# Performance work log

Hardware: AMD Instinct MI355X
Metric: run time of the kernel (lower is better)

## Reference

```python
import jax, jax.numpy as jnp
import numpy as np

TOP_K = 2  # num_activated_experts

def setup_inputs() -> dict:
    key = jax.random.key(0)
    kx, kg, k1, k2, k3 = jax.random.split(key, 5)
    B, S, H, I, E = 2, 2048, 1024, 2048, 8
    scale = 0.02
    return {
        "x": jax.random.normal(kx, (B, S, H), dtype=jnp.float32),
        "gate_w": jax.random.normal(kg, (E, H), dtype=jnp.float32) * scale,   # router Linear weight [E,H]
        "w_gate": jax.random.normal(k1, (E, H, I), dtype=jnp.float32) * scale, # gate_proj per expert
        "w_up":   jax.random.normal(k2, (E, H, I), dtype=jnp.float32) * scale, # up_proj per expert
        "w_down": jax.random.normal(k3, (E, I, H), dtype=jnp.float32) * scale, # down_proj per expert
    }

def reference(x, gate_w, w_gate, w_up, w_down):
    B, S, H = x.shape
    E = gate_w.shape[0]
    T = B * S
    xf = x.reshape(T, H)
    # router
    router_logits = xf @ gate_w.T                                  # [T,E]
    probs = jax.nn.softmax(router_logits.astype(jnp.float32), axis=-1)
    top_w, top_i = jax.lax.top_k(probs, TOP_K)                      # [T,K]
    top_w = top_w / jnp.sum(top_w, axis=-1, keepdims=True)
    top_w = top_w.astype(x.dtype)
    # dense combine weights: w[t,e] = routing weight if expert e selected, else 0
    w = jnp.zeros((T, E), dtype=x.dtype).at[jnp.arange(T)[:, None], top_i].add(top_w)
    # experts (SwiGLU), computed densely over experts, masked by combine weights
    g = jnp.einsum('th,ehi->tei', xf, w_gate)                       # [T,E,I]
    u = jnp.einsum('th,ehi->tei', xf, w_up)                         # [T,E,I]
    h = jax.nn.silu(g) * u
    y = jnp.einsum('tei,eih->teh', h, w_down)                       # [T,E,H]
    out = jnp.einsum('teh,te->th', y, w)                            # weighted combine
    return out.reshape(B, S, H), router_logits
```

## Files before the change

kernel.cpp:

```cpp
#include <hip/hip_runtime.h>
#include <hip/hip_bf16.h>
#include <math.h>

#define T_TOK 4096
#define H_DIM 1024
#define I_DIM 2048
#define E_NUM 8

typedef __bf16 bf16x8 __attribute__((ext_vector_type(8)));
typedef float  f32x4  __attribute__((ext_vector_type(4)));
typedef unsigned short u16x4 __attribute__((ext_vector_type(4)));
typedef unsigned short u16x8 __attribute__((ext_vector_type(8)));

__device__ inline void gll16(const void* g, void* l) {
    __builtin_amdgcn_global_load_lds(
        (const __attribute__((address_space(1))) void*)g,
        (__attribute__((address_space(3))) void*)l, 16, 0, 0);
}

__device__ inline unsigned short f2bf(float f) {
    union { float f; unsigned u; } v; v.f = f;
    unsigned r = v.u + 0x7FFF + ((v.u >> 16) & 1);
    return (unsigned short)(r >> 16);
}

__device__ inline void stage_tile64(const unsigned short* gbase, size_t stride_elems,
                                    int k0, char* smbase, int tid, int wv) {
#pragma unroll
    for (int it = 0; it < 4; ++it) {
        int idx = it * 256 + tid;
        int r   = idx >> 3;
        int kg  = (idx & 7) ^ (r & 7);
        const void* g = gbase + (size_t)r * stride_elems + k0 + kg * 8;
        void* l = smbase + it * 4096 + wv * 1024;
        gll16(g, l);
    }
}

__device__ inline bf16x8 frag_ld64(const char* smbase, int row, int kg_log) {
    int kg = kg_log ^ (row & 7);
    return *(const bf16x8*)(smbase + row * 128 + kg * 16);
}

__global__ __launch_bounds__(256) void router_kernel(
    const float* __restrict__ x, const float* __restrict__ gw,
    float* __restrict__ logits_out, int* __restrict__ te, float2* __restrict__ tw)
{
    int wave = threadIdx.x >> 6;
    int lane = threadIdx.x & 63;
    int t = blockIdx.x * 4 + wave;
    if (t >= T_TOK) return;

    float xs[16];
#pragma unroll
    for (int i = 0; i < 16; ++i) xs[i] = x[(size_t)t * H_DIM + i * 64 + lane];

    float lg[E_NUM];
#pragma unroll
    for (int e = 0; e < E_NUM; ++e) {
        float acc = 0.f;
#pragma unroll
        for (int i = 0; i < 16; ++i) acc += xs[i] * gw[e * H_DIM + i * 64 + lane];
#pragma unroll
        for (int off = 32; off >= 1; off >>= 1) acc += __shfl_xor(acc, off, 64);
        lg[e] = acc;
    }

    if (lane == 0) {
#pragma unroll
        for (int e = 0; e < E_NUM; ++e) logits_out[(size_t)t * E_NUM + e] = lg[e];
        float m = lg[0];
        for (int e = 1; e < E_NUM; ++e) m = fmaxf(m, lg[e]);
        float p[E_NUM]; float s = 0.f;
        for (int e = 0; e < E_NUM; ++e) { p[e] = expf(lg[e] - m); s += p[e]; }
        float invs = 1.f / s;
        for (int e = 0; e < E_NUM; ++e) p[e] *= invs;
        int i0 = 0; float p0 = p[0];
        for (int e = 1; e < E_NUM; ++e) if (p[e] > p0) { p0 = p[e]; i0 = e; }
        int i1 = -1; float p1 = -1.f;
        for (int e = 0; e < E_NUM; ++e) { if (e == i0) continue; if (p[e] > p1) { p1 = p[e]; i1 = e; } }
        float inv = 1.f / (p0 + p1);
        te[t] = i0 | (i1 << 4);
        tw[t] = make_float2(p0 * inv, p1 * inv);
    }
}

__global__ __launch_bounds__(256) void scan_kernel(
    const int* __restrict__ te, const float2* __restrict__ tw,
    int* __restrict__ counts, int* __restrict__ tok_list,
    float* __restrict__ w_list, int* __restrict__ tslot)
{
    int e = blockIdx.x;
    int tid = threadIdx.x, lane = tid & 63, wv = tid >> 6;

    int    pk[16];
    float2 w2[16];
#pragma unroll
    for (int c = 0; c < 16; ++c) pk[c] = te[c * 256 + tid];
#pragma unroll
    for (int c = 0; c < 16; ++c) w2[c] = tw[c * 256 + tid];

    __shared__ int wbase[4];
    int running = 0;
#pragma unroll
    for (int c = 0; c < 16; ++c) {
        int t  = c * 256 + tid;
        int e0 = pk[c] & 15, e1 = pk[c] >> 4;
        bool f0 = (e0 == e), f1 = (e1 == e);
        bool f  = f0 || f1;
        unsigned long long b = __ballot(f);
        int pre = __popcll(b & ((1ull << lane) - 1ull));
        if (lane == 0) wbase[wv] = __popcll(b);
        __syncthreads();
        int base = running;
#pragma unroll
        for (int w = 0; w < 4; ++w) if (w < wv) base += wbase[w];
        int tot = wbase[0] + wbase[1] + wbase[2] + wbase[3];
        if (f) {
            int pos = base + pre;
            tok_list[e * T_TOK + pos] = t;
            w_list[e * T_TOK + pos]   = f0 ? w2[c].x : w2[c].y;
            tslot[t * 2 + (f0 ? 0 : 1)] = e * T_TOK + pos;
        }
        running += tot;
        __syncthreads();
    }
    if (tid == 0) counts[e] = running;
}

__global__ void offsets_kernel(const int* __restrict__ counts, int* __restrict__ poff)
{
    if (threadIdx.x == 0 && blockIdx.x == 0) {
        int s = 0;
        for (int e = 0; e < E_NUM; ++e) { poff[e] = s; s += ((counts[e] + 127) >> 7) << 7; }
    }
}

__global__ __launch_bounds__(256) void gather_x(
    const float* __restrict__ x, const int* __restrict__ counts,
    const int* __restrict__ poff, const int* __restrict__ tok_list,
    unsigned short* __restrict__ xg)
{
    int e  = blockIdx.x >> 7;
    int mt = blockIdx.x & 127;
    int cnt = counts[e];
    int padded = (cnt + 127) & ~127;
    int m0 = mt * 32;
    if (m0 >= padded) return;
    int base = poff[e];
#pragma unroll 4
    for (int it = 0; it < 32; ++it) {
        int idx = it * 256 + threadIdx.x;
        int r  = idx >> 8;
        int c4 = idx & 255;
        int m  = m0 + r;
        int mc = (m < cnt) ? m : cnt - 1;
        int t  = tok_list[e * T_TOK + mc];
        float4 v = *(const float4*)(x + (size_t)t * H_DIM + c4 * 4);
        u16x4 o;
        o[0] = f2bf(v.x); o[1] = f2bf(v.y); o[2] = f2bf(v.z); o[3] = f2bf(v.w);
        *(u16x4*)(xg + (size_t)(base + m) * H_DIM + c4 * 4) = o;
    }
}

__global__ __launch_bounds__(256) void transpose_cvt(
    const float* __restrict__ in, unsigned short* __restrict__ out, int K, int N)
{
    int e = blockIdx.z;
    in  += (size_t)e * K * N;
    out += (size_t)e * K * N;
    int k0 = blockIdx.y * 64, n0 = blockIdx.x * 64;
    __shared__ float t[64][65];
#pragma unroll
    for (int it = 0; it < 4; ++it) {
        int idx = it * 256 + threadIdx.x;
        int r = idx >> 4, c4 = idx & 15;
        float4 v = *(const float4*)(in + (size_t)(k0 + r) * N + n0 + c4 * 4);
        t[r][c4 * 4 + 0] = v.x; t[r][c4 * 4 + 1] = v.y;
        t[r][c4 * 4 + 2] = v.z; t[r][c4 * 4 + 3] = v.w;
    }
    __syncthreads();
#pragma unroll
    for (int it = 0; it < 2; ++it) {
        int slot = it * 256 + threadIdx.x;
        int n = slot >> 3, kg = slot & 7;
        u16x8 o;
#pragma unroll
        for (int j = 0; j < 8; ++j) o[j] = f2bf(t[kg * 8 + j][n]);
        *(u16x8*)(out + (size_t)(n0 + n) * K + k0 + kg * 8) = o;
    }
}

__global__ __launch_bounds__(256, 2) void mlp1_kernel(
    const unsigned short* __restrict__ xg,
    const unsigned short* __restrict__ wgT, const unsigned short* __restrict__ wuT,
    const int* __restrict__ counts, const int* __restrict__ poff,
    unsigned short* __restrict__ hbuf)
{
    int e = blockIdx.z;
    int cnt = counts[e];
    int m0 = blockIdx.y * 128;
    if (m0 >= cnt) return;
    int n0 = blockIdx.x * 128;

    const unsigned short* A  = xg  + (size_t)(poff[e] + m0) * H_DIM;
    const unsigned short* Bg = wgT + (size_t)e * I_DIM * H_DIM + (size_t)n0 * H_DIM;
    const unsigned short* Bu = wuT + (size_t)e * I_DIM * H_DIM + (size_t)n0 * H_DIM;

    __shared__ char sm[49152];
    char* sA  = sm;
    char* sBg = sm + 16384;
    char* sBu = sm + 32768;

    int tid = threadIdx.x, lane = tid & 63, wv = tid >> 6;
    int wm = (wv >> 1) * 64, wn = (wv & 1) * 64;
    int q = lane >> 4, rl = lane & 15;

    f32x4 accg[4][4], accu[4][4];
#pragma unroll
    for (int i = 0; i < 4; ++i)
#pragma unroll
        for (int j = 0; j < 4; ++j) { accg[i][j] = (f32x4){0.f,0.f,0.f,0.f}; accu[i][j] = (f32x4){0.f,0.f,0.f,0.f}; }

    for (int k0 = 0; k0 < H_DIM; k0 += 64) {
        stage_tile64(A,  H_DIM, k0, sA,  tid, wv);
        stage_tile64(Bg, H_DIM, k0, sBg, tid, wv);
        stage_tile64(Bu, H_DIM, k0, sBu, tid, wv);
        __syncthreads();

#pragma unroll
        for (int h = 0; h < 2; ++h) {
            bf16x8 af[4], bgf[4], bu2[4];
#pragma unroll
            for (int i = 0; i < 4; ++i) af[i]  = frag_ld64(sA,  wm + i * 16 + rl, h * 4 + q);
#pragma unroll
            for (int j = 0; j < 4; ++j) { bgf[j] = frag_ld64(sBg, wn + j * 16 + rl, h * 4 + q);
                                          bu2[j] = frag_ld64(sBu, wn + j * 16 + rl, h * 4 + q); }
#pragma unroll
            for (int i = 0; i < 4; ++i)
#pragma unroll
                for (int j = 0; j < 4; ++j) {
                    accg[i][j] = __builtin_amdgcn_mfma_f32_16x16x32_bf16(af[i], bgf[j], accg[i][j], 0, 0, 0);
                    accu[i][j] = __builtin_amdgcn_mfma_f32_16x16x32_bf16(af[i], bu2[j], accu[i][j], 0, 0, 0);
                }
        }
        __syncthreads();
    }

    size_t hrow0 = (size_t)(poff[e] + m0);
#pragma unroll
    for (int i = 0; i < 4; ++i)
#pragma unroll
        for (int p = 0; p < 4; ++p) {
            int row = wm + i * 16 + q * 4 + p;
            unsigned short* orow = hbuf + (hrow0 + row) * I_DIM + n0 + wn + rl;
#pragma unroll
            for (int j = 0; j < 4; ++j) {
                float g = accg[i][j][p], u = accu[i][j][p];
                float hv = g / (1.f + __expf(-g)) * u;
                orow[j * 16] = f2bf(hv);
            }
        }
}

__global__ __launch_bounds__(256, 2) void mlp2_kernel(
    const unsigned short* __restrict__ hbuf,
    const unsigned short* __restrict__ wdT,
    const int* __restrict__ counts, const int* __restrict__ poff,
    float* __restrict__ ybuf)
{
    int e = blockIdx.z;
    int cnt = counts[e];
    int m0 = blockIdx.y * 128;
    if (m0 >= cnt) return;
    int n0 = blockIdx.x * 128;

    const unsigned short* A = hbuf + (size_t)(poff[e] + m0) * I_DIM;
    const unsigned short* B = wdT  + (size_t)e * H_DIM * I_DIM + (size_t)n0 * I_DIM;

    __shared__ char sm[32768];
    char* sA = sm;
    char* sB = sm + 16384;

    int tid = threadIdx.x, lane = tid & 63, wv = tid >> 6;
    int wm = (wv >> 1) * 64, wn = (wv & 1) * 64;
    int q = lane >> 4, rl = lane & 15;

    f32x4 acc[4][4];
#pragma unroll
    for (int i = 0; i < 4; ++i)
#pragma unroll
        for (int j = 0; j < 4; ++j) acc[i][j] = (f32x4){0.f,0.f,0.f,0.f};

    for (int k0 = 0; k0 < I_DIM; k0 += 64) {
        stage_tile64(A, I_DIM, k0, sA, tid, wv);
        stage_tile64(B, I_DIM, k0, sB, tid, wv);
        __syncthreads();

#pragma unroll
        for (int h = 0; h < 2; ++h) {
            bf16x8 af[4], bf[4];
#pragma unroll
            for (int i = 0; i < 4; ++i) af[i] = frag_ld64(sA, wm + i * 16 + rl, h * 4 + q);
#pragma unroll
            for (int j = 0; j < 4; ++j) bf[j] = frag_ld64(sB, wn + j * 16 + rl, h * 4 + q);
#pragma unroll
            for (int i = 0; i < 4; ++i)
#pragma unroll
                for (int j = 0; j < 4; ++j)
                    acc[i][j] = __builtin_amdgcn_mfma_f32_16x16x32_bf16(af[i], bf[j], acc[i][j], 0, 0, 0);
        }
        __syncthreads();
    }

    size_t yrow0 = (size_t)(poff[e] + m0);
#pragma unroll
    for (int i = 0; i < 4; ++i)
#pragma unroll
        for (int p = 0; p < 4; ++p) {
            int row = wm + i * 16 + q * 4 + p;
            float* op = ybuf + (yrow0 + row) * H_DIM + n0 + wn + rl;
#pragma unroll
            for (int j = 0; j < 4; ++j) op[j * 16] = acc[i][j][p];
        }
}

__global__ __launch_bounds__(256) void combine_kernel(
    const float* __restrict__ ybuf, const int* __restrict__ poff,
    const int* __restrict__ tslot, const float* __restrict__ w_list,
    float* __restrict__ out)
{
    int t  = blockIdx.x;
    int c4 = threadIdx.x;
    int s0 = tslot[t * 2 + 0], s1 = tslot[t * 2 + 1];
    float w0 = w_list[s0], w1 = w_list[s1];
    int e0 = s0 >> 12, p0 = s0 & 4095;
    int e1 = s1 >> 12, p1 = s1 & 4095;
    size_t r0 = (size_t)(poff[e0] + p0) * H_DIM;
    size_t r1 = (size_t)(poff[e1] + p1) * H_DIM;
    float4 a = *(const float4*)(ybuf + r0 + c4 * 4);
    float4 b = *(const float4*)(ybuf + r1 + c4 * 4);
    float4 o;
    o.x = w0 * a.x + w1 * b.x;
    o.y = w0 * a.y + w1 * b.y;
    o.z = w0 * a.z + w1 * b.z;
    o.w = w0 * a.w + w1 * b.w;
    *(float4*)(out + (size_t)t * H_DIM + c4 * 4) = o;
}

extern "C" void kernel_launch(void* const* d_in, const int* in_sizes, int n_in,
                              void* d_out, int out_size, void* d_ws, size_t ws_size,
                              hipStream_t stream)
{
    const float* x      = (const float*)d_in[0];
    const float* gate_w = (const float*)d_in[1];
    const float* w_gate = (const float*)d_in[2];
    const float* w_up   = (const float*)d_in[3];
    const float* w_down = (const float*)d_in[4];

    float* out        = (float*)d_out;
    float* logits_out = out + (size_t)T_TOK * H_DIM;

    char* ws = (char*)d_ws;
    int*   counts   = (int*)ws;
    int*   poff     = (int*)(ws + 64);
    int*   tok_list = (int*)(ws + 1024);
    float* w_list   = (float*)(ws + 1024 + E_NUM * T_TOK * 4);
    int*   tslot    = (int*)(ws + 1024 + 2 * E_NUM * T_TOK * 4);
    int*   te       = (int*)(ws + 1024 + 2 * E_NUM * T_TOK * 4 + 2 * T_TOK * 4);
    float2* tw      = (float2*)(ws + 1024 + 2 * E_NUM * T_TOK * 4 + 3 * T_TOK * 4);

    const size_t XG_ROWS = 9216;
    const size_t OFF_XG = 1u << 20;
    const size_t OFF_HB = OFF_XG + XG_ROWS * H_DIM * 2;
    const size_t OFF_WG = OFF_HB + XG_ROWS * I_DIM * 2;
    const size_t OFF_WU = OFF_WG + (size_t)E_NUM * H_DIM * I_DIM * 2;
    const size_t OFF_WD = OFF_WU + (size_t)E_NUM * H_DIM * I_DIM * 2;

    unsigned short* xg   = (unsigned short*)(ws + OFF_XG);
    unsigned short* hbuf = (unsigned short*)(ws + OFF_HB);
    unsigned short* wgT  = (unsigned short*)(ws + OFF_WG);
    unsigned short* wuT  = (unsigned short*)(ws + OFF_WU);
    unsigned short* wdT  = (unsigned short*)(ws + OFF_WD);
    float* ybuf = (float*)(ws + OFF_WG);

    router_kernel<<<T_TOK / 4, 256, 0, stream>>>(x, gate_w, logits_out, te, tw);
    scan_kernel<<<E_NUM, 256, 0, stream>>>(te, tw, counts, tok_list, w_list, tslot);
    offsets_kernel<<<1, 64, 0, stream>>>(counts, poff);

    dim3 gt1(I_DIM / 64, H_DIM / 64, E_NUM);
    transpose_cvt<<<gt1, 256, 0, stream>>>(w_gate, wgT, H_DIM, I_DIM);
    transpose_cvt<<<gt1, 256, 0, stream>>>(w_up,   wuT, H_DIM, I_DIM);
    dim3 gt2(H_DIM / 64, I_DIM / 64, E_NUM);
    transpose_cvt<<<gt2, 256, 0, stream>>>(w_down, wdT, I_DIM, H_DIM);

    gather_x<<<E_NUM * 128, 256, 0, stream>>>(x, counts, poff, tok_list, xg);

    dim3 g1(I_DIM / 128, T_TOK / 128, E_NUM);
    mlp1_kernel<<<g1, 256, 0, stream>>>(xg, wgT, wuT, counts, poff, hbuf);

    dim3 g2(H_DIM / 128, T_TOK / 128, E_NUM);
    mlp2_kernel<<<g2, 256, 0, stream>>>(hbuf, wdT, counts, poff, ybuf);

    combine_kernel<<<T_TOK, 256, 0, stream>>>(ybuf, poff, tslot, w_list, out);
}
```

Baseline: 417.2 us.

## Double-buffer LDS staging and widen expert GEMM tiles to 128x256 with 512 threads

Both expert GEMM kernels now use a two-stage LDS ping-pong with a K-step of 32. The next tile's global-to-LDS loads are issued before the MFMA work on the current tile, so load latency overlaps compute and only one barrier is needed per step. Block tiles grow from 128x128 to 128x256 with 8 waves, which raises reuse of the A tile. In exchange, LDS use is larger (80KB for mlp1), which may reduce occupancy, and the grid has fewer blocks, which may hurt load balance across the uneven per-expert counts.

Measured after the change: 440.5 us. 5.6% more time.

```diff
diff --git a/kernel.cpp b/kernel.cpp
--- a/kernel.cpp
+++ b/kernel.cpp
@@ -24,22 +24,26 @@
     return (unsigned short)(r >> 16);
 }
 
-__device__ inline void stage_tile64(const unsigned short* gbase, size_t stride_elems,
-                                    int k0, char* smbase, int tid, int wv) {
-#pragma unroll
-    for (int it = 0; it < 4; ++it) {
-        int idx = it * 256 + tid;
-        int r   = idx >> 3;
-        int kg  = (idx & 7) ^ (r & 7);
-        const void* g = gbase + (size_t)r * stride_elems + k0 + kg * 8;
-        void* l = smbase + it * 4096 + wv * 1024;
-        gll16(g, l);
-    }
-}
-
-__device__ inline bf16x8 frag_ld64(const char* smbase, int row, int kg_log) {
-    int kg = kg_log ^ (row & 7);
-    return *(const bf16x8*)(smbase + row * 128 + kg * 16);
+__device__ inline void stage_a32(const unsigned short* gbase, size_t stride, int k0,
+                                 char* dst, int tid, int wv) {
+    int r  = tid >> 2;
+    int kg = (tid & 3) ^ (r & 3);
+    gll16(gbase + (size_t)r * stride + k0 + kg * 8, dst + wv * 1024);
+}
+__device__ inline void stage_b32(const unsigned short* gbase, size_t stride, int k0,
+                                 char* dst, int tid, int wv) {
+#pragma unroll
+    for (int it = 0; it < 2; ++it) {
+        int idx = it * 512 + tid;
+        int r  = idx >> 2;
+        int kg = (idx & 3) ^ (r & 3);
+        gll16(gbase + (size_t)r * stride + k0 + kg * 8, dst + it * 8192 + wv * 1024);
+    }
+}
+
+__device__ inline bf16x8 frag_ld32(const char* smbase, int row, int q) {
+    int kg = q ^ (row & 3);
+    return *(const bf16x8*)(smbase + row * 64 + kg * 16);
 }
 
 __global__ __launch_bounds__(256) void router_kernel(
@@ -191,7 +195,7 @@
     }
 }
 
-__global__ __launch_bounds__(256, 2) void mlp1_kernel(
+__global__ __launch_bounds__(512, 2) void mlp1_kernel(
     const unsigned short* __restrict__ xg,
     const unsigned short* __restrict__ wgT, const unsigned short* __restrict__ wuT,
     const int* __restrict__ counts, const int* __restrict__ poff,
@@ -201,19 +205,16 @@
     int cnt = counts[e];
     int m0 = blockIdx.y * 128;
     if (m0 >= cnt) return;
-    int n0 = blockIdx.x * 128;
+    int n0 = blockIdx.x * 256;
 
     const unsigned short* A  = xg  + (size_t)(poff[e] + m0) * H_DIM;
     const unsigned short* Bg = wgT + (size_t)e * I_DIM * H_DIM + (size_t)n0 * H_DIM;
     const unsigned short* Bu = wuT + (size_t)e * I_DIM * H_DIM + (size_t)n0 * H_DIM;
 
-    __shared__ char sm[49152];
-    char* sA  = sm;
-    char* sBg = sm + 16384;
-    char* sBu = sm + 32768;
+    __shared__ char sm[81920];
 
     int tid = threadIdx.x, lane = tid & 63, wv = tid >> 6;
-    int wm = (wv >> 1) * 64, wn = (wv & 1) * 64;
+    int wm = (wv >> 2) * 64, wn = (wv & 3) * 64;
     int q = lane >> 4, rl = lane & 15;
 
     f32x4 accg[4][4], accu[4][4];
@@ -222,29 +223,42 @@
 #pragma unroll
         for (int j = 0; j < 4; ++j) { accg[i][j] = (f32x4){0.f,0.f,0.f,0.f}; accu[i][j] = (f32x4){0.f,0.f,0.f,0.f}; }
 
-    for (int k0 = 0; k0 < H_DIM; k0 += 64) {
-        stage_tile64(A,  H_DIM, k0, sA,  tid, wv);
-        stage_tile64(Bg, H_DIM, k0, sBg, tid, wv);
-        stage_tile64(Bu, H_DIM, k0, sBu, tid, wv);
+    const int NST = H_DIM / 32;
+    stage_a32(A,  H_DIM, 0, sm,         tid, wv);
+    stage_b32(Bg, H_DIM, 0, sm + 8192,  tid, wv);
+    stage_b32(Bu, H_DIM, 0, sm + 24576, tid, wv);
+    __syncthreads();
+
+    int cur = 0;
+    for (int ks = 0; ks < NST; ++ks) {
+        int nxt = cur ^ 1;
+        if (ks + 1 < NST) {
+            int k0 = (ks + 1) * 32;
+            char* nb = sm + nxt * 40960;
+            stage_a32(A,  H_DIM, k0, nb,         tid, wv);
+            stage_b32(Bg, H_DIM, k0, nb + 8192,  tid, wv);
+            stage_b32(Bu, H_DIM, k0, nb + 24576, tid, wv);
+        }
+        const char* cb  = sm + cur * 40960;
+        const char* sA  = cb;
+        const char* sBg = cb + 8192;
+        const char* sBu = cb + 24576;
+
+        bf16x8 af[4], bgf[4], bu2[4];
+#pragma unroll
+        for (int i = 0; i < 4; ++i) af[i]  = frag_ld32(sA,  wm + i * 16 + rl, q);
+#pragma unroll
+        for (int j = 0; j < 4; ++j) { bgf[j] = frag_ld32(sBg, wn + j * 16 + rl, q);
+                                      bu2[j] = frag_ld32(sBu, wn + j * 16 + rl, q); }
+#pragma unroll
+        for (int i = 0; i < 4; ++i)
+#pragma unroll
+            for (int j = 0; j < 4; ++j) {
+                accg[i][j] = __builtin_amdgcn_mfma_f32_16x16x32_bf16(af[i], bgf[j], accg[i][j], 0, 0, 0);
+                accu[i][j] = __builtin_amdgcn_mfma_f32_16x16x32_bf16(af[i], bu2[j], accu[i][j], 0, 0, 0);
+            }
         __syncthreads();
-
-#pragma unroll
-        for (int h = 0; h < 2; ++h) {
-            bf16x8 af[4], bgf[4], bu2[4];
-#pragma unroll
-            for (int i = 0; i < 4; ++i) af[i]  = frag_ld64(sA,  wm + i * 16 + rl, h * 4 + q);
-#pragma unroll
-            for (int j = 0; j < 4; ++j) { bgf[j] = frag_ld64(sBg, wn + j * 16 + rl, h * 4 + q);
-                                          bu2[j] = frag_ld64(sBu, wn + j * 16 + rl, h * 4 + q); }
-#pragma unroll
-            for (int i = 0; i < 4; ++i)
-#pragma unroll
-                for (int j = 0; j < 4; ++j) {
-                    accg[i][j] = __builtin_amdgcn_mfma_f32_16x16x32_bf16(af[i], bgf[j], accg[i][j], 0, 0, 0);
-                    accu[i][j] = __builtin_amdgcn_mfma_f32_16x16x32_bf16(af[i], bu2[j], accu[i][j], 0, 0, 0);
-                }
-        }
-        __syncthreads();
+        cur = nxt;
     }
 
     size_t hrow0 = (size_t)(poff[e] + m0);
@@ -263,7 +277,7 @@
         }
 }
 
-__global__ __launch_bounds__(256, 2) void mlp2_kernel(
+__global__ __launch_bounds__(512, 4) void mlp2_kernel(
     const unsigned short* __restrict__ hbuf,
     const unsigned short* __restrict__ wdT,
     const int* __restrict__ counts, const int* __restrict__ poff,
@@ -273,17 +287,15 @@
     int cnt = counts[e];
     int m0 = blockIdx.y * 128;
     if (m0 >= cnt) return;
-    int n0 = blockIdx.x * 128;
+    int n0 = blockIdx.x * 256;
 
     const unsigned short* A = hbuf + (size_t)(poff[e] + m0) * I_DIM;
     const unsigned short* B = wdT  + (size_t)e * H_DIM * I_DIM + (size_t)n0 * I_DIM;
 
-    __shared__ char sm[32768];
-    char* sA = sm;
-    char* sB = sm + 16384;
+    __shared__ char sm[49152];
 
     int tid = threadIdx.x, lane = tid & 63, wv = tid >> 6;
-    int wm = (wv >> 1) * 64, wn = (wv & 1) * 64;
+    int wm = (wv >> 2) * 64, wn = (wv & 3) * 64;
     int q = lane >> 4, rl = lane & 15;
 
     f32x4 acc[4][4];
@@ -292,25 +304,36 @@
 #pragma unroll
         for (int j = 0; j < 4; ++j) acc[i][j] = (f32x4){0.f,0.f,0.f,0.f};
 
-    for (int k0 = 0; k0 < I_DIM; k0 += 64) {
-        stage_tile64(A, I_DIM, k0, sA, tid, wv);
-        stage_tile64(B, I_DIM, k0, sB, tid, wv);
+    const int NST = I_DIM / 32;
+    stage_a32(A, I_DIM, 0, sm,        tid, wv);
+    stage_b32(B, I_DIM, 0, sm + 8192, tid, wv);
+    __syncthreads();
+
+    int cur = 0;
+    for (int ks = 0; ks < NST; ++ks) {
+        int nxt = cur ^ 1;
+        if (ks + 1 < NST) {
+            int k0 = (ks + 1) * 32;
+            char* nb = sm + nxt * 24576;
+            stage_a32(A, I_DIM, k0, nb,        tid, wv);
+            stage_b32(B, I_DIM, k0, nb + 8192, tid, wv);
+        }
+        const char* cb = sm + cur * 24576;
+        const char* sA = cb;
+        const char* sB = cb + 8192;
+
+        bf16x8 af[4], bf[4];
+#pragma unroll
+        for (int i = 0; i < 4; ++i) af[i] = frag_ld32(sA, wm + i * 16 + rl, q);
+#pragma unroll
+        for (int j = 0; j < 4; ++j) bf[j] = frag_ld32(sB, wn + j * 16 + rl, q);
+#pragma unroll
+        for (int i = 0; i < 4; ++i)
+#pragma unroll
+            for (int j = 0; j < 4; ++j)
+                acc[i][j] = __builtin_amdgcn_mfma_f32_16x16x32_bf16(af[i], bf[j], acc[i][j], 0, 0, 0);
         __syncthreads();
-
-#pragma unroll
-        for (int h = 0; h < 2; ++h) {
-            bf16x8 af[4], bf[4];
-#pragma unroll
-            for (int i = 0; i < 4; ++i) af[i] = frag_ld64(sA, wm + i * 16 + rl, h * 4 + q);
-#pragma unroll
-            for (int j = 0; j < 4; ++j) bf[j] = frag_ld64(sB, wn + j * 16 + rl, h * 4 + q);
-#pragma unroll
-            for (int i = 0; i < 4; ++i)
-#pragma unroll
-                for (int j = 0; j < 4; ++j)
-                    acc[i][j] = __builtin_amdgcn_mfma_f32_16x16x32_bf16(af[i], bf[j], acc[i][j], 0, 0, 0);
-        }
-        __syncthreads();
+        cur = nxt;
     }
 
     size_t yrow0 = (size_t)(poff[e] + m0);
@@ -396,11 +419,11 @@
 
     gather_x<<<E_NUM * 128, 256, 0, stream>>>(x, counts, poff, tok_list, xg);
 
-    dim3 g1(I_DIM / 128, T_TOK / 128, E_NUM);
-    mlp1_kernel<<<g1, 256, 0, stream>>>(xg, wgT, wuT, counts, poff, hbuf);
-
-    dim3 g2(H_DIM / 128, T_TOK / 128, E_NUM);
-    mlp2_kernel<<<g2, 256, 0, stream>>>(hbuf, wdT, counts, poff, ybuf);
+    dim3 g1(I_DIM / 256, T_TOK / 128, E_NUM);
+    mlp1_kernel<<<g1, 512, 0, stream>>>(xg, wgT, wuT, counts, poff, hbuf);
+
+    dim3 g2(H_DIM / 256, T_TOK / 128, E_NUM);
+    mlp2_kernel<<<g2, 512, 0, stream>>>(hbuf, wdT, counts, poff, ybuf);
 
     combine_kernel<<<T_TOK, 256, 0, stream>>>(ybuf, poff, tslot, w_list, out);
 }
```
